# Optimization experiments

Hardware: AMD Instinct MI355X
Metric: run time of the kernel (lower is better)

The kernel has to match this reference:

```python
import jax, jax.numpy as jnp
import numpy as np

EMBED_DIM = 1024
NUM_HEADS = 16
HEAD_DIM = EMBED_DIM // NUM_HEADS
R = 8
ALPHA = 32
SCALING = ALPHA / R


def setup_inputs() -> dict:
    key = jax.random.key(0)
    ks = jax.random.split(key, 12)
    d = EMBED_DIM
    s = 1.0 / np.sqrt(d)
    inp = {
        "x": jax.random.normal(ks[0], (4, 2048, d), dtype=jnp.float32),
        # base linear weights (torch layout: [out, in]) and biases
        "Wq": jax.random.normal(ks[1], (d, d), dtype=jnp.float32) * s,
        "bq": jax.random.normal(ks[2], (d,), dtype=jnp.float32) * s,
        "Wk": jax.random.normal(ks[3], (d, d), dtype=jnp.float32) * s,
        "bk": jax.random.normal(ks[4], (d,), dtype=jnp.float32) * s,
        "Wv": jax.random.normal(ks[5], (d, d), dtype=jnp.float32) * s,
        "bv": jax.random.normal(ks[6], (d,), dtype=jnp.float32) * s,
        "Wo": jax.random.normal(ks[7], (d, d), dtype=jnp.float32) * s,
        "bo": jax.random.normal(ks[8], (d,), dtype=jnp.float32) * s,
        # LoRA adapters for q and v: A [r, in], B [out, r]
        "Aq": jax.random.normal(ks[9], (R, d), dtype=jnp.float32) * s,
        "Bq": jnp.zeros((d, R), dtype=jnp.float32),
        "Av": jax.random.normal(ks[10], (R, d), dtype=jnp.float32) * s,
        "Bv": jnp.zeros((d, R), dtype=jnp.float32),
    }
    return inp


def _lora_linear(x, W, b, A, Bm):
    # base: x @ W.T + b ; lora: scaling * (x @ A.T) @ B.T
    return x @ W.T + b + SCALING * ((x @ A.T) @ Bm.T)


def reference(x, Wq, bq, Wk, bk, Wv, bv, Wo, bo, Aq, Bq, Av, Bv):
    B, T, C = x.shape
    H, D = NUM_HEADS, HEAD_DIM
    q = _lora_linear(x, Wq, bq, Aq, Bq)
    k = x @ Wk.T + bk
    v = _lora_linear(x, Wv, bv, Av, Bv)
    # [B, T, C] -> [B, H, T, D]
    q = q.reshape(B, T, H, D).transpose(0, 2, 1, 3)
    k = k.reshape(B, T, H, D).transpose(0, 2, 1, 3)
    v = v.reshape(B, T, H, D).transpose(0, 2, 1, 3)
    scores = jnp.einsum("bhqd,bhkd->bhqk", q, k) / np.sqrt(D).astype(np.float32)
    weights = jax.nn.softmax(scores, axis=-1)
    out = jnp.einsum("bhqk,bhkd->bhqd", weights, v)
    out = out.transpose(0, 2, 1, 3).reshape(B, T, C)
    return out @ Wo.T + bo
```

## Files before the change

### kernel.cpp

```cpp
#include <hip/hip_runtime.h>
#include <hip/hip_bf16.h>
#include <stdint.h>

namespace {
constexpr int kB = 4, kT = 2048, kC = 1024, kH = 16, kD = 64;
constexpr int kM = kB * kT;
constexpr int kR = 8;
constexpr float kScaling = 4.0f;
constexpr float kInvSqrtD = 0.125f;
}

typedef short short8 __attribute__((ext_vector_type(8)));
typedef float f32x4 __attribute__((ext_vector_type(4)));
typedef unsigned short ushort4v __attribute__((ext_vector_type(4)));
typedef unsigned short ushort8v __attribute__((ext_vector_type(8)));

__device__ inline uint32_t f32_to_bf16_rne(float f) {
  uint32_t u = __float_as_uint(f);
  return (u + 0x7fffu + ((u >> 16) & 1u)) >> 16;
}

__device__ inline void split4(const float4 v, ushort4v& h, ushort4v& l) {
  const float f[4] = {v.x, v.y, v.z, v.w};
#pragma unroll
  for (int j = 0; j < 4; ++j) {
    const uint32_t hb = f32_to_bf16_rne(f[j]);
    const float hf = __uint_as_float(hb << 16);
    const uint32_t lb = f32_to_bf16_rne(f[j] - hf);
    h[j] = (unsigned short)hb;
    l[j] = (unsigned short)lb;
  }
}

__device__ inline short8 pack8(ushort4v a, ushort4v b) {
  short8 r;
  r[0] = (short)a[0]; r[1] = (short)a[1]; r[2] = (short)a[2]; r[3] = (short)a[3];
  r[4] = (short)b[0]; r[5] = (short)b[1]; r[6] = (short)b[2]; r[7] = (short)b[3];
  return r;
}

__global__ __launch_bounds__(256) void lora_xa_kernel(
    const float* __restrict__ x, const float* __restrict__ Aq,
    const float* __restrict__ Av, float* __restrict__ xa) {
  const int wave = threadIdx.x >> 6;
  const int lane = threadIdx.x & 63;
  const int row = (blockIdx.x << 2) + wave;
  const float4* xr = reinterpret_cast<const float4*>(x) + (size_t)row * (kC / 4);
  const float4* aq = reinterpret_cast<const float4*>(Aq);
  const float4* av = reinterpret_cast<const float4*>(Av);
  float acc[16];
#pragma unroll
  for (int r = 0; r < 16; ++r) acc[r] = 0.f;
#pragma unroll
  for (int jj = 0; jj < (kC / 4) / 64; ++jj) {
    const int j = lane + jj * 64;
    const float4 xv = xr[j];
#pragma unroll
    for (int r = 0; r < 8; ++r) {
      const float4 a = aq[r * (kC / 4) + j];
      acc[r] += xv.x * a.x + xv.y * a.y + xv.z * a.z + xv.w * a.w;
      const float4 b = av[r * (kC / 4) + j];
      acc[8 + r] += xv.x * b.x + xv.y * b.y + xv.z * b.z + xv.w * b.w;
    }
  }
#pragma unroll
  for (int r = 0; r < 16; ++r) {
    float v = acc[r];
#pragma unroll
    for (int off = 32; off > 0; off >>= 1) v += __shfl_xor(v, off, 64);
    if (lane == 0) xa[(size_t)row * 16 + r] = v;
  }
}

__global__ __launch_bounds__(256, 2) void gemm_bf16x3_kernel(
    const float* __restrict__ X, const float* __restrict__ W,
    const float* __restrict__ bias, const float* __restrict__ xa,
    const float* __restrict__ Bm, float* __restrict__ out,
    const int lora_sel ,
    const int out_mode) {
  constexpr int BK = 32;
  __shared__ __align__(16) unsigned char sA[128 * 128];
  __shared__ __align__(16) unsigned char sB[128 * 128];

  const int tid = threadIdx.x;
  const int m0 = blockIdx.y << 7;
  const int n0 = blockIdx.x << 7;
  const int wave = tid >> 6, lane = tid & 63;
  const int wr = wave >> 1, wc = wave & 1;
  const int lrow = lane & 15;
  const int lkg = lane >> 4;

  const int r0 = tid >> 3;
  const int c4 = (tid & 7) << 2;
  const float* xbase = X + (size_t)(m0 + r0) * kC + c4;
  const float* wbase = W + (size_t)(n0 + r0) * kC + c4;
  const int ch = c4 >> 3;
  const int slot = (c4 & 7) << 1;

  f32x4 acc[4][4];
#pragma unroll
  for (int a = 0; a < 4; ++a)
#pragma unroll
    for (int b = 0; b < 4; ++b) acc[a][b] = (f32x4){0.f, 0.f, 0.f, 0.f};

  float4 ga[4], gb[4];
#pragma unroll
  for (int i = 0; i < 4; ++i) {
    ga[i] = *reinterpret_cast<const float4*>(xbase + (size_t)i * 32 * kC);
    gb[i] = *reinterpret_cast<const float4*>(wbase + (size_t)i * 32 * kC);
  }

  for (int k0 = 0; k0 < kC; k0 += BK) {
#pragma unroll
    for (int i = 0; i < 4; ++i) {
      const int r = r0 + 32 * i;
      const int rbase = r * 128;
      const int s7 = r & 7;
      ushort4v ha, la, hb2, lb2;
      split4(ga[i], ha, la);
      split4(gb[i], hb2, lb2);
      *reinterpret_cast<ushort4v*>(&sA[rbase + ((ch ^ s7) << 4) + slot]) = ha;
      *reinterpret_cast<ushort4v*>(&sA[rbase + (((ch | 4) ^ s7) << 4) + slot]) = la;
      *reinterpret_cast<ushort4v*>(&sB[rbase + ((ch ^ s7) << 4) + slot]) = hb2;
      *reinterpret_cast<ushort4v*>(&sB[rbase + (((ch | 4) ^ s7) << 4) + slot]) = lb2;
    }
    __syncthreads();

    if (k0 + BK < kC) {
#pragma unroll
      for (int i = 0; i < 4; ++i) {
        ga[i] = *reinterpret_cast<const float4*>(xbase + (k0 + BK) + (size_t)i * 32 * kC);
        gb[i] = *reinterpret_cast<const float4*>(wbase + (k0 + BK) + (size_t)i * 32 * kC);
      }
    }

    short8 ah[4], al[4];
#pragma unroll
    for (int rb = 0; rb < 4; ++rb) {
      const int rA = wr * 64 + rb * 16 + lrow;
      ah[rb] = *reinterpret_cast<const short8*>(&sA[rA * 128 + ((lkg ^ (rA & 7)) << 4)]);
      al[rb] = *reinterpret_cast<const short8*>(&sA[rA * 128 + (((lkg | 4) ^ (rA & 7)) << 4)]);
    }
#pragma unroll
    for (int cb = 0; cb < 4; ++cb) {
      const int rB = wc * 64 + cb * 16 + lrow;
      const short8 bhf = *reinterpret_cast<const short8*>(&sB[rB * 128 + ((lkg ^ (rB & 7)) << 4)]);
      const short8 blf = *reinterpret_cast<const short8*>(&sB[rB * 128 + (((lkg | 4) ^ (rB & 7)) << 4)]);
#pragma unroll
      for (int rb = 0; rb < 4; ++rb) {
        acc[rb][cb] = __builtin_amdgcn_mfma_f32_16x16x32_bf16(ah[rb], bhf, acc[rb][cb], 0, 0, 0);
        acc[rb][cb] = __builtin_amdgcn_mfma_f32_16x16x32_bf16(ah[rb], blf, acc[rb][cb], 0, 0, 0);
        acc[rb][cb] = __builtin_amdgcn_mfma_f32_16x16x32_bf16(al[rb], bhf, acc[rb][cb], 0, 0, 0);
      }
    }
    __syncthreads();
  }

#pragma unroll
  for (int rb = 0; rb < 4; ++rb) {
    const int mbase = m0 + wr * 64 + rb * 16 + (lkg << 2);
    float la2[4][kR];
    if (lora_sel >= 0) {
#pragma unroll
      for (int i = 0; i < 4; ++i)
#pragma unroll
        for (int r = 0; r < kR; ++r)
          la2[i][r] = xa[(size_t)(mbase + i) * 16 + lora_sel + r];
    }
#pragma unroll
    for (int cb = 0; cb < 4; ++cb) {
      const int n = n0 + wc * 64 + cb * 16 + lrow;
      const float bi = bias[n];
      float vv[4];
#pragma unroll
      for (int i = 0; i < 4; ++i) {
        vv[i] = acc[rb][cb][i] + bi;
        if (lora_sel >= 0) {
          float lv = 0.f;
#pragma unroll
          for (int r = 0; r < kR; ++r)
            lv = fmaf(la2[i][r], Bm[(size_t)n * kR + r], lv);
          vv[i] += kScaling * lv;
        }
      }
      if (out_mode == 2) {
        const int bb_ = mbase >> 11;
        const int t0 = mbase & (kT - 1);
        const int hh = n >> 6;
        const int dd = n & (kD - 1);
        *reinterpret_cast<float4*>(
            out + (((size_t)bb_ * kH + hh) * kD + dd) * kT + t0) =
            make_float4(vv[0], vv[1], vv[2], vv[3]);
      } else if (out_mode == 1) {
#pragma unroll
        for (int i = 0; i < 4; ++i) {
          const int m = mbase + i;
          const int bb_ = m >> 11;
          const int t = m & (kT - 1);
          const int hh = n >> 6;
          const int dd = n & (kD - 1);
          out[(((size_t)bb_ * kH + hh) * kT + t) * kD + dd] = vv[i];
        }
      } else {
#pragma unroll
        for (int i = 0; i < 4; ++i)
          out[(size_t)(mbase + i) * kC + n] = vv[i];
      }
    }
  }
}

__global__ __launch_bounds__(256) void attn_mfma_kernel(
    const float* __restrict__ q, const float* __restrict__ k,
    const float* __restrict__ vT, float* __restrict__ ctx) {
  __shared__ __align__(16) unsigned char sKh[64 * 128];
  __shared__ __align__(16) unsigned char sKl[64 * 128];
  __shared__ __align__(16) unsigned char sVt[64 * 128];
  __shared__ __align__(16) unsigned char sP[128 * 128];

  const int tid = threadIdx.x;
  const int wave = tid >> 6, lane = tid & 63;
  const int lrow = lane & 15, lg = lane >> 4;
  const int bh = blockIdx.y;
  const int q0 = blockIdx.x << 7;
  const int b = bh >> 4, h = bh & 15;

  const float* qbh = q + (size_t)bh * kT * kD;
  const float* kbh = k + (size_t)bh * kT * kD;

  const int srow = tid >> 2;
  const int scq = (tid & 3) << 4;
  const float* kstage = kbh + (size_t)srow * kD + scq;
  const float* vstage = vT + ((size_t)bh * kD + srow) * kT + scq;

  short8 qh[2][2], ql[2][2];
#pragma unroll
  for (int qs = 0; qs < 2; ++qs)
#pragma unroll
    for (int d0 = 0; d0 < 2; ++d0) {
      const int qrow = q0 + wave * 32 + qs * 16 + lrow;
      const float* qp2 = qbh + (size_t)qrow * kD + d0 * 32 + lg * 8;
      float4 f0 = *reinterpret_cast<const float4*>(qp2);
      float4 f1 = *reinterpret_cast<const float4*>(qp2 + 4);
      f0.x *= kInvSqrtD; f0.y *= kInvSqrtD; f0.z *= kInvSqrtD; f0.w *= kInvSqrtD;
      f1.x *= kInvSqrtD; f1.y *= kInvSqrtD; f1.z *= kInvSqrtD; f1.w *= kInvSqrtD;
      ushort4v h0, l0, h1, l1;
      split4(f0, h0, l0);
      split4(f1, h1, l1);
      qh[qs][d0] = pack8(h0, h1);
      ql[qs][d0] = pack8(l0, l1);
    }

  f32x4 acc_o[2][4];
#pragma unroll
  for (int qs = 0; qs < 2; ++qs)
#pragma unroll
    for (int dr = 0; dr < 4; ++dr) acc_o[qs][dr] = (f32x4){0.f, 0.f, 0.f, 0.f};
  float m_i[2] = {-3.0e38f, -3.0e38f};
  float l_i[2] = {0.f, 0.f};

  constexpr int kNT = kT / 64;
  float4 kpre[4], vpre[4];
#pragma unroll
  for (int i = 0; i < 4; ++i) {
    kpre[i] = *reinterpret_cast<const float4*>(kstage + i * 4);
    vpre[i] = *reinterpret_cast<const float4*>(vstage + i * 4);
  }

  for (int kt = 0; kt < kNT; ++kt) {
    {
      const int s7k = srow & 7;
#pragma unroll
      for (int half = 0; half < 2; ++half) {
        ushort4v h0, l0, h1, l1;
        split4(kpre[2 * half], h0, l0);
        split4(kpre[2 * half + 1], h1, l1);
        const int chk = ((scq >> 3) + half) ^ s7k;
        *reinterpret_cast<ushort8v*>(&sKh[srow * 128 + (chk << 4)]) =
            (ushort8v){h0[0], h0[1], h0[2], h0[3], h1[0], h1[1], h1[2], h1[3]};
        *reinterpret_cast<ushort8v*>(&sKl[srow * 128 + (chk << 4)]) =
            (ushort8v){l0[0], l0[1], l0[2], l0[3], l1[0], l1[1], l1[2], l1[3]};
        ushort8v w;
        const float vf0[8] = {vpre[2 * half].x, vpre[2 * half].y,
                              vpre[2 * half].z, vpre[2 * half].w,
                              vpre[2 * half + 1].x, vpre[2 * half + 1].y,
                              vpre[2 * half + 1].z, vpre[2 * half + 1].w};
#pragma unroll
        for (int e = 0; e < 8; ++e) w[e] = (unsigned short)f32_to_bf16_rne(vf0[e]);
        *reinterpret_cast<ushort8v*>(&sVt[srow * 128 + (chk << 4)]) = w;
      }
    }
    __syncthreads();

    if (kt + 1 < kNT) {
      const int knext = (kt + 1) << 6;
#pragma unroll
      for (int i = 0; i < 4; ++i) {
        kpre[i] = *reinterpret_cast<const float4*>(kstage + (size_t)knext * kD + i * 4);
        vpre[i] = *reinterpret_cast<const float4*>(vstage + knext + i * 4);
      }
    }

    f32x4 acc_s[2][4];
#pragma unroll
    for (int qs = 0; qs < 2; ++qs)
#pragma unroll
      for (int kvr = 0; kvr < 4; ++kvr) acc_s[qs][kvr] = (f32x4){0.f, 0.f, 0.f, 0.f};
#pragma unroll
    for (int d0 = 0; d0 < 2; ++d0) {
#pragma unroll
      for (int kvr = 0; kvr < 4; ++kvr) {
        const int rk = kvr * 16 + lrow;
        const int byt = rk * 128 + ((((d0 << 2) + lg) ^ (rk & 7)) << 4);
        const short8 khf = *reinterpret_cast<const short8*>(&sKh[byt]);
        const short8 klf = *reinterpret_cast<const short8*>(&sKl[byt]);
#pragma unroll
        for (int qs = 0; qs < 2; ++qs) {
          acc_s[qs][kvr] = __builtin_amdgcn_mfma_f32_16x16x32_bf16(khf, qh[qs][d0], acc_s[qs][kvr], 0, 0, 0);
          acc_s[qs][kvr] = __builtin_amdgcn_mfma_f32_16x16x32_bf16(khf, ql[qs][d0], acc_s[qs][kvr], 0, 0, 0);
          acc_s[qs][kvr] = __builtin_amdgcn_mfma_f32_16x16x32_bf16(klf, qh[qs][d0], acc_s[qs][kvr], 0, 0, 0);
        }
      }
    }

#pragma unroll
    for (int qs = 0; qs < 2; ++qs) {
      float mx = acc_s[qs][0][0];
#pragma unroll
      for (int kvr = 0; kvr < 4; ++kvr)
#pragma unroll
        for (int i = 0; i < 4; ++i) mx = fmaxf(mx, acc_s[qs][kvr][i]);
      mx = fmaxf(mx, __shfl_xor(mx, 16, 64));
      mx = fmaxf(mx, __shfl_xor(mx, 32, 64));
      const float mnew = fmaxf(m_i[qs], mx);
      const float alpha = __expf(m_i[qs] - mnew);
      m_i[qs] = mnew;
      const int prow = wave * 32 + qs * 16 + lrow;
      const int p7 = prow & 7;
      float rs = 0.f;
#pragma unroll
      for (int kvr = 0; kvr < 4; ++kvr) {
        ushort4v pu;
#pragma unroll
        for (int i = 0; i < 4; ++i) {
          const float pv = __expf(acc_s[qs][kvr][i] - mnew);
          rs += pv;
          pu[i] = (unsigned short)f32_to_bf16_rne(pv);
        }
        const int chunk = ((kvr << 1) + (lg >> 1)) ^ p7;
        *reinterpret_cast<ushort4v*>(&sP[prow * 128 + (chunk << 4) + ((lg & 1) << 3)]) = pu;
      }
      rs += __shfl_xor(rs, 16, 64);
      rs += __shfl_xor(rs, 32, 64);
      l_i[qs] = l_i[qs] * alpha + rs;
#pragma unroll
      for (int dr = 0; dr < 4; ++dr)
#pragma unroll
        for (int i = 0; i < 4; ++i) acc_o[qs][dr][i] *= alpha;
    }
    __builtin_amdgcn_sched_barrier(0);

#pragma unroll
    for (int ks = 0; ks < 2; ++ks) {
      short8 pf[2];
#pragma unroll
      for (int qs = 0; qs < 2; ++qs) {
        const int prow = wave * 32 + qs * 16 + lrow;
        pf[qs] = *reinterpret_cast<const short8*>(
            &sP[prow * 128 + ((((ks << 2) + lg) ^ (prow & 7)) << 4)]);
      }
#pragma unroll
      for (int dr = 0; dr < 4; ++dr) {
        const int rv = dr * 16 + lrow;
        const short8 vf = *reinterpret_cast<const short8*>(
            &sVt[rv * 128 + ((((ks << 2) + lg) ^ (rv & 7)) << 4)]);
        acc_o[0][dr] = __builtin_amdgcn_mfma_f32_16x16x32_bf16(vf, pf[0], acc_o[0][dr], 0, 0, 0);
        acc_o[1][dr] = __builtin_amdgcn_mfma_f32_16x16x32_bf16(vf, pf[1], acc_o[1][dr], 0, 0, 0);
      }
    }
    __syncthreads();
  }

#pragma unroll
  for (int qs = 0; qs < 2; ++qs) {
    const float inv = 1.0f / l_i[qs];
    const int qq = q0 + wave * 32 + qs * 16 + lrow;
    float* op = ctx + ((size_t)b * kT + qq) * kC + (h << 6);
#pragma unroll
    for (int dr = 0; dr < 4; ++dr) {
      const float4 o4 = make_float4(acc_o[qs][dr][0] * inv, acc_o[qs][dr][1] * inv,
                                    acc_o[qs][dr][2] * inv, acc_o[qs][dr][3] * inv);
      *reinterpret_cast<float4*>(op + dr * 16 + (lg << 2)) = o4;
    }
  }
}

extern "C" void kernel_launch(void* const* d_in, const int* in_sizes, int n_in,
                              void* d_out, int out_size, void* d_ws, size_t ws_size,
                              hipStream_t stream) {
  const float* x  = (const float*)d_in[0];
  const float* Wq = (const float*)d_in[1];
  const float* bq = (const float*)d_in[2];
  const float* Wk = (const float*)d_in[3];
  const float* bk = (const float*)d_in[4];
  const float* Wv = (const float*)d_in[5];
  const float* bv = (const float*)d_in[6];
  const float* Wo = (const float*)d_in[7];
  const float* bo = (const float*)d_in[8];
  const float* Aq = (const float*)d_in[9];
  const float* Bq = (const float*)d_in[10];
  const float* Av = (const float*)d_in[11];
  const float* Bv = (const float*)d_in[12];
  float* out = (float*)d_out;

  float* ws = (float*)d_ws;
  float* qb  = ws;
  float* kb  = qb  + (size_t)kM * kC;
  float* vbT = kb  + (size_t)kM * kC;
  float* ctx = vbT + (size_t)kM * kC;
  float* xa  = ctx + (size_t)kM * kC;

  hipLaunchKernelGGL(lora_xa_kernel, dim3(kM / 4), dim3(256), 0, stream,
                     x, Aq, Av, xa);

  const dim3 gg(kC / 128, kM / 128);
  hipLaunchKernelGGL(gemm_bf16x3_kernel, gg, dim3(256), 0, stream,
                     x, Wq, bq, xa, Bq, qb, 0, 1);
  hipLaunchKernelGGL(gemm_bf16x3_kernel, gg, dim3(256), 0, stream,
                     x, Wk, bk, nullptr, nullptr, kb, -1, 1);
  hipLaunchKernelGGL(gemm_bf16x3_kernel, gg, dim3(256), 0, stream,
                     x, Wv, bv, xa, Bv, vbT, 8, 2);

  hipLaunchKernelGGL(attn_mfma_kernel, dim3(kT / 128, kB * kH), dim3(256), 0, stream,
                     qb, kb, vbT, ctx);

  hipLaunchKernelGGL(gemm_bf16x3_kernel, gg, dim3(256), 0, stream,
                     ctx, Wo, bo, nullptr, nullptr, out, -1, 0);
}
```

Measured before the change: 641.1 us.

## Pre-split operands into bf16 hi/lo planes and store intermediates as bf16

Adds a pack kernel that splits x and all four weight matrices into bf16 high/low planes once per call. The GEMMs and attention then load those planes directly instead of converting fp32 tiles inside their main loops. Q/K/V and the attention context are written as bf16 planes, which halves or keeps intermediate traffic and removes in-loop splitting. The softmax is folded into exp2 with the log2e factor baked into the Q scale, and P is packed with hardware bf16 conversions. The cost is extra pack passes over x and the weights, plus a larger workspace.

Measured after the change: 710.5 us. 1.11x slower.

```diff
diff --git a/kernel.cpp b/kernel.cpp
--- a/kernel.cpp
+++ b/kernel.cpp
@@ -7,36 +7,54 @@
 constexpr int kM = kB * kT;
 constexpr int kR = 8;
 constexpr float kScaling = 4.0f;
-constexpr float kInvSqrtD = 0.125f;
+constexpr float kQScale = 0.125f * 1.4426950408889634f;
 }
 
 typedef short short8 __attribute__((ext_vector_type(8)));
 typedef float f32x4 __attribute__((ext_vector_type(4)));
 typedef unsigned short ushort4v __attribute__((ext_vector_type(4)));
 typedef unsigned short ushort8v __attribute__((ext_vector_type(8)));
-
-__device__ inline uint32_t f32_to_bf16_rne(float f) {
-  uint32_t u = __float_as_uint(f);
-  return (u + 0x7fffu + ((u >> 16) & 1u)) >> 16;
-}
-
-__device__ inline void split4(const float4 v, ushort4v& h, ushort4v& l) {
-  const float f[4] = {v.x, v.y, v.z, v.w};
-#pragma unroll
-  for (int j = 0; j < 4; ++j) {
-    const uint32_t hb = f32_to_bf16_rne(f[j]);
-    const float hf = __uint_as_float(hb << 16);
-    const uint32_t lb = f32_to_bf16_rne(f[j] - hf);
-    h[j] = (unsigned short)hb;
-    l[j] = (unsigned short)lb;
-  }
-}
-
-__device__ inline short8 pack8(ushort4v a, ushort4v b) {
-  short8 r;
-  r[0] = (short)a[0]; r[1] = (short)a[1]; r[2] = (short)a[2]; r[3] = (short)a[3];
-  r[4] = (short)b[0]; r[5] = (short)b[1]; r[6] = (short)b[2]; r[7] = (short)b[3];
-  return r;
+typedef unsigned int uint2v __attribute__((ext_vector_type(2)));
+
+__device__ inline unsigned short bf16_bits(float f) {
+  __hip_bfloat16 h = __float2bfloat16(f);
+  unsigned short u;
+  __builtin_memcpy(&u, &h, 2);
+  return u;
+}
+__device__ inline float bits_f(unsigned short u) {
+  return __uint_as_float((uint32_t)u << 16);
+}
+__device__ inline void split1(float f, unsigned short& h, unsigned short& l) {
+  h = bf16_bits(f);
+  l = bf16_bits(f - bits_f(h));
+}
+__device__ inline uint32_t cvtpk2(float a, float b) {
+  __hip_bfloat162 h2 = __float22bfloat162_rn(float2{a, b});
+  uint32_t u;
+  __builtin_memcpy(&u, &h2, 4);
+  return u;
+}
+
+__global__ __launch_bounds__(256) void pack_kernel(
+    const float* __restrict__ s, unsigned short* __restrict__ hp,
+    unsigned short* __restrict__ lp, int n4) {
+  int i = blockIdx.x * 256 + threadIdx.x;
+  const int stride = gridDim.x * 256;
+  for (; i < n4; i += stride) {
+    const float4 v = reinterpret_cast<const float4*>(s)[i];
+    const float f[4] = {v.x, v.y, v.z, v.w};
+    ushort4v h, l;
+#pragma unroll
+    for (int j = 0; j < 4; ++j) {
+      unsigned short hb, lb;
+      split1(f[j], hb, lb);
+      h[j] = hb;
+      l[j] = lb;
+    }
+    reinterpret_cast<ushort4v*>(hp)[i] = h;
+    reinterpret_cast<ushort4v*>(lp)[i] = l;
+  }
 }
 
 __global__ __launch_bounds__(256) void lora_xa_kernel(
@@ -72,12 +90,14 @@
   }
 }
 
-__global__ __launch_bounds__(256, 2) void gemm_bf16x3_kernel(
-    const float* __restrict__ X, const float* __restrict__ W,
+__global__ __launch_bounds__(256, 2) void gemm_planes_kernel(
+    const unsigned short* __restrict__ Ah_g, const unsigned short* __restrict__ Al_g,
+    const unsigned short* __restrict__ Bh_g, const unsigned short* __restrict__ Bl_g,
     const float* __restrict__ bias, const float* __restrict__ xa,
-    const float* __restrict__ Bm, float* __restrict__ out,
-    const int lora_sel ,
-    const int out_mode) {
+    const float* __restrict__ Bm,
+    unsigned short* __restrict__ o16a, unsigned short* __restrict__ o16b,
+    float* __restrict__ o32,
+    const int lora_sel, const int out_mode, const float out_scale) {
   constexpr int BK = 32;
   __shared__ __align__(16) unsigned char sA[128 * 128];
   __shared__ __align__(16) unsigned char sB[128 * 128];
@@ -90,12 +110,12 @@
   const int lrow = lane & 15;
   const int lkg = lane >> 4;
 
-  const int r0 = tid >> 3;
-  const int c4 = (tid & 7) << 2;
-  const float* xbase = X + (size_t)(m0 + r0) * kC + c4;
-  const float* wbase = W + (size_t)(n0 + r0) * kC + c4;
-  const int ch = c4 >> 3;
-  const int slot = (c4 & 7) << 1;
+  const int srow = tid >> 1;
+  const int sc0 = (tid & 1) << 1;
+  const unsigned short* pa_h = Ah_g + (size_t)(m0 + srow) * kC + sc0 * 8;
+  const unsigned short* pa_l = Al_g + (size_t)(m0 + srow) * kC + sc0 * 8;
+  const unsigned short* pb_h = Bh_g + (size_t)(n0 + srow) * kC + sc0 * 8;
+  const unsigned short* pb_l = Bl_g + (size_t)(n0 + srow) * kC + sc0 * 8;
 
   f32x4 acc[4][4];
 #pragma unroll
@@ -103,34 +123,36 @@
 #pragma unroll
     for (int b = 0; b < 4; ++b) acc[a][b] = (f32x4){0.f, 0.f, 0.f, 0.f};
 
-  float4 ga[4], gb[4];
-#pragma unroll
-  for (int i = 0; i < 4; ++i) {
-    ga[i] = *reinterpret_cast<const float4*>(xbase + (size_t)i * 32 * kC);
-    gb[i] = *reinterpret_cast<const float4*>(wbase + (size_t)i * 32 * kC);
+  ushort8v rah[2], ral[2], rbh[2], rbl[2];
+#pragma unroll
+  for (int j = 0; j < 2; ++j) {
+    rah[j] = *reinterpret_cast<const ushort8v*>(pa_h + j * 8);
+    ral[j] = *reinterpret_cast<const ushort8v*>(pa_l + j * 8);
+    rbh[j] = *reinterpret_cast<const ushort8v*>(pb_h + j * 8);
+    rbl[j] = *reinterpret_cast<const ushort8v*>(pb_l + j * 8);
   }
 
   for (int k0 = 0; k0 < kC; k0 += BK) {
-#pragma unroll
-    for (int i = 0; i < 4; ++i) {
-      const int r = r0 + 32 * i;
-      const int rbase = r * 128;
-      const int s7 = r & 7;
-      ushort4v ha, la, hb2, lb2;
-      split4(ga[i], ha, la);
-      split4(gb[i], hb2, lb2);
-      *reinterpret_cast<ushort4v*>(&sA[rbase + ((ch ^ s7) << 4) + slot]) = ha;
-      *reinterpret_cast<ushort4v*>(&sA[rbase + (((ch | 4) ^ s7) << 4) + slot]) = la;
-      *reinterpret_cast<ushort4v*>(&sB[rbase + ((ch ^ s7) << 4) + slot]) = hb2;
-      *reinterpret_cast<ushort4v*>(&sB[rbase + (((ch | 4) ^ s7) << 4) + slot]) = lb2;
+    const int rbase = srow * 128;
+    const int s7 = srow & 7;
+#pragma unroll
+    for (int j = 0; j < 2; ++j) {
+      const int c = sc0 + j;
+      *reinterpret_cast<ushort8v*>(&sA[rbase + ((c ^ s7) << 4)]) = rah[j];
+      *reinterpret_cast<ushort8v*>(&sA[rbase + (((c | 4) ^ s7) << 4)]) = ral[j];
+      *reinterpret_cast<ushort8v*>(&sB[rbase + ((c ^ s7) << 4)]) = rbh[j];
+      *reinterpret_cast<ushort8v*>(&sB[rbase + (((c | 4) ^ s7) << 4)]) = rbl[j];
     }
     __syncthreads();
 
     if (k0 + BK < kC) {
-#pragma unroll
-      for (int i = 0; i < 4; ++i) {
-        ga[i] = *reinterpret_cast<const float4*>(xbase + (k0 + BK) + (size_t)i * 32 * kC);
-        gb[i] = *reinterpret_cast<const float4*>(wbase + (k0 + BK) + (size_t)i * 32 * kC);
+      const int kn = k0 + BK;
+#pragma unroll
+      for (int j = 0; j < 2; ++j) {
+        rah[j] = *reinterpret_cast<const ushort8v*>(pa_h + kn + j * 8);
+        ral[j] = *reinterpret_cast<const ushort8v*>(pa_l + kn + j * 8);
+        rbh[j] = *reinterpret_cast<const ushort8v*>(pb_h + kn + j * 8);
+        rbl[j] = *reinterpret_cast<const ushort8v*>(pb_l + kn + j * 8);
       }
     }
 
@@ -182,37 +204,45 @@
             lv = fmaf(la2[i][r], Bm[(size_t)n * kR + r], lv);
           vv[i] += kScaling * lv;
         }
-      }
-      if (out_mode == 2) {
+        vv[i] *= out_scale;
+      }
+      if (out_mode == 1) {
         const int bb_ = mbase >> 11;
         const int t0 = mbase & (kT - 1);
         const int hh = n >> 6;
         const int dd = n & (kD - 1);
-        *reinterpret_cast<float4*>(
-            out + (((size_t)bb_ * kH + hh) * kD + dd) * kT + t0) =
-            make_float4(vv[0], vv[1], vv[2], vv[3]);
-      } else if (out_mode == 1) {
 #pragma unroll
         for (int i = 0; i < 4; ++i) {
-          const int m = mbase + i;
-          const int bb_ = m >> 11;
-          const int t = m & (kT - 1);
-          const int hh = n >> 6;
-          const int dd = n & (kD - 1);
-          out[(((size_t)bb_ * kH + hh) * kT + t) * kD + dd] = vv[i];
+          const size_t off = (((size_t)bb_ * kH + hh) * kT + t0 + i) * kD + dd;
+          unsigned short hb, lb;
+          split1(vv[i], hb, lb);
+          o16a[off] = hb;
+          o16b[off] = lb;
         }
+      } else if (out_mode == 2) {
+        const int bb_ = mbase >> 11;
+        const int t0 = mbase & (kT - 1);
+        const int hh = n >> 6;
+        const int dd = n & (kD - 1);
+        ushort4v w;
+#pragma unroll
+        for (int i = 0; i < 4; ++i) w[i] = bf16_bits(vv[i]);
+        *reinterpret_cast<ushort4v*>(
+            o16a + (((size_t)bb_ * kH + hh) * kD + dd) * kT + t0) = w;
       } else {
 #pragma unroll
         for (int i = 0; i < 4; ++i)
-          out[(size_t)(mbase + i) * kC + n] = vv[i];
+          o32[(size_t)(mbase + i) * kC + n] = vv[i];
       }
     }
   }
 }
 
 __global__ __launch_bounds__(256) void attn_mfma_kernel(
-    const float* __restrict__ q, const float* __restrict__ k,
-    const float* __restrict__ vT, float* __restrict__ ctx) {
+    const unsigned short* __restrict__ Qh, const unsigned short* __restrict__ Ql,
+    const unsigned short* __restrict__ Kh_g, const unsigned short* __restrict__ Kl_g,
+    const unsigned short* __restrict__ Vt_g,
+    unsigned short* __restrict__ ctx_h, unsigned short* __restrict__ ctx_l) {
   __shared__ __align__(16) unsigned char sKh[64 * 128];
   __shared__ __align__(16) unsigned char sKl[64 * 128];
   __shared__ __align__(16) unsigned char sVt[64 * 128];
@@ -225,31 +255,22 @@
   const int q0 = blockIdx.x << 7;
   const int b = bh >> 4, h = bh & 15;
 
-  const float* qbh = q + (size_t)bh * kT * kD;
-  const float* kbh = k + (size_t)bh * kT * kD;
+  short8 qh[2][2], ql[2][2];
+#pragma unroll
+  for (int qs = 0; qs < 2; ++qs)
+#pragma unroll
+    for (int d0 = 0; d0 < 2; ++d0) {
+      const size_t off =
+          ((size_t)bh * kT + q0 + wave * 32 + qs * 16 + lrow) * kD + d0 * 32 + lg * 8;
+      qh[qs][d0] = *reinterpret_cast<const short8*>(Qh + off);
+      ql[qs][d0] = *reinterpret_cast<const short8*>(Ql + off);
+    }
 
   const int srow = tid >> 2;
-  const int scq = (tid & 3) << 4;
-  const float* kstage = kbh + (size_t)srow * kD + scq;
-  const float* vstage = vT + ((size_t)bh * kD + srow) * kT + scq;
-
-  short8 qh[2][2], ql[2][2];
-#pragma unroll
-  for (int qs = 0; qs < 2; ++qs)
-#pragma unroll
-    for (int d0 = 0; d0 < 2; ++d0) {
-      const int qrow = q0 + wave * 32 + qs * 16 + lrow;
-      const float* qp2 = qbh + (size_t)qrow * kD + d0 * 32 + lg * 8;
-      float4 f0 = *reinterpret_cast<const float4*>(qp2);
-      float4 f1 = *reinterpret_cast<const float4*>(qp2 + 4);
-      f0.x *= kInvSqrtD; f0.y *= kInvSqrtD; f0.z *= kInvSqrtD; f0.w *= kInvSqrtD;
-      f1.x *= kInvSqrtD; f1.y *= kInvSqrtD; f1.z *= kInvSqrtD; f1.w *= kInvSqrtD;
-      ushort4v h0, l0, h1, l1;
-      split4(f0, h0, l0);
-      split4(f1, h1, l1);
-      qh[qs][d0] = pack8(h0, h1);
-      ql[qs][d0] = pack8(l0, l1);
-    }
+  const int sc0 = (tid & 3) << 1;
+  const unsigned short* khs = Kh_g + ((size_t)bh * kT + srow) * kD + sc0 * 8;
+  const unsigned short* kls = Kl_g + ((size_t)bh * kT + srow) * kD + sc0 * 8;
+  const unsigned short* vts = Vt_g + ((size_t)bh * kD + srow) * kT + sc0 * 8;
 
   f32x4 acc_o[2][4];
 #pragma unroll
@@ -260,44 +281,36 @@
   float l_i[2] = {0.f, 0.f};
 
   constexpr int kNT = kT / 64;
-  float4 kpre[4], vpre[4];
-#pragma unroll
-  for (int i = 0; i < 4; ++i) {
-    kpre[i] = *reinterpret_cast<const float4*>(kstage + i * 4);
-    vpre[i] = *reinterpret_cast<const float4*>(vstage + i * 4);
+  ushort8v kph[2], kpl[2], vpv[2];
+#pragma unroll
+  for (int j = 0; j < 2; ++j) {
+    kph[j] = *reinterpret_cast<const ushort8v*>(khs + j * 8);
+    kpl[j] = *reinterpret_cast<const ushort8v*>(kls + j * 8);
+    vpv[j] = *reinterpret_cast<const ushort8v*>(vts + j * 8);
   }
 
   for (int kt = 0; kt < kNT; ++kt) {
     {
-      const int s7k = srow & 7;
-#pragma unroll
-      for (int half = 0; half < 2; ++half) {
-        ushort4v h0, l0, h1, l1;
-        split4(kpre[2 * half], h0, l0);
-        split4(kpre[2 * half + 1], h1, l1);
-        const int chk = ((scq >> 3) + half) ^ s7k;
-        *reinterpret_cast<ushort8v*>(&sKh[srow * 128 + (chk << 4)]) =
-            (ushort8v){h0[0], h0[1], h0[2], h0[3], h1[0], h1[1], h1[2], h1[3]};
-        *reinterpret_cast<ushort8v*>(&sKl[srow * 128 + (chk << 4)]) =
-            (ushort8v){l0[0], l0[1], l0[2], l0[3], l1[0], l1[1], l1[2], l1[3]};
-        ushort8v w;
-        const float vf0[8] = {vpre[2 * half].x, vpre[2 * half].y,
-                              vpre[2 * half].z, vpre[2 * half].w,
-                              vpre[2 * half + 1].x, vpre[2 * half + 1].y,
-                              vpre[2 * half + 1].z, vpre[2 * half + 1].w};
-#pragma unroll
-        for (int e = 0; e < 8; ++e) w[e] = (unsigned short)f32_to_bf16_rne(vf0[e]);
-        *reinterpret_cast<ushort8v*>(&sVt[srow * 128 + (chk << 4)]) = w;
+      const int rb2 = srow * 128;
+      const int s7 = srow & 7;
+#pragma unroll
+      for (int j = 0; j < 2; ++j) {
+        const int c = sc0 + j;
+        *reinterpret_cast<ushort8v*>(&sKh[rb2 + ((c ^ s7) << 4)]) = kph[j];
+        *reinterpret_cast<ushort8v*>(&sKl[rb2 + ((c ^ s7) << 4)]) = kpl[j];
+        *reinterpret_cast<ushort8v*>(&sVt[rb2 + ((c ^ s7) << 4)]) = vpv[j];
       }
     }
     __syncthreads();
 
     if (kt + 1 < kNT) {
-      const int knext = (kt + 1) << 6;
-#pragma unroll
-      for (int i = 0; i < 4; ++i) {
-        kpre[i] = *reinterpret_cast<const float4*>(kstage + (size_t)knext * kD + i * 4);
-        vpre[i] = *reinterpret_cast<const float4*>(vstage + knext + i * 4);
+      const size_t koffK = (size_t)(kt + 1) * 64 * kD;
+      const int koffV = (kt + 1) * 64;
+#pragma unroll
+      for (int j = 0; j < 2; ++j) {
+        kph[j] = *reinterpret_cast<const ushort8v*>(khs + koffK + j * 8);
+        kpl[j] = *reinterpret_cast<const ushort8v*>(kls + koffK + j * 8);
+        vpv[j] = *reinterpret_cast<const ushort8v*>(vts + koffV + j * 8);
       }
     }
 
@@ -333,22 +346,24 @@
       mx = fmaxf(mx, __shfl_xor(mx, 16, 64));
       mx = fmaxf(mx, __shfl_xor(mx, 32, 64));
       const float mnew = fmaxf(m_i[qs], mx);
-      const float alpha = __expf(m_i[qs] - mnew);
+      const float alpha = __builtin_exp2f(m_i[qs] - mnew);
       m_i[qs] = mnew;
       const int prow = wave * 32 + qs * 16 + lrow;
       const int p7 = prow & 7;
       float rs = 0.f;
 #pragma unroll
       for (int kvr = 0; kvr < 4; ++kvr) {
-        ushort4v pu;
+        float p[4];
 #pragma unroll
         for (int i = 0; i < 4; ++i) {
-          const float pv = __expf(acc_s[qs][kvr][i] - mnew);
-          rs += pv;
-          pu[i] = (unsigned short)f32_to_bf16_rne(pv);
+          p[i] = __builtin_exp2f(acc_s[qs][kvr][i] - mnew);
+          rs += p[i];
         }
+        uint2v pu;
+        pu[0] = cvtpk2(p[0], p[1]);
+        pu[1] = cvtpk2(p[2], p[3]);
         const int chunk = ((kvr << 1) + (lg >> 1)) ^ p7;
-        *reinterpret_cast<ushort4v*>(&sP[prow * 128 + (chunk << 4) + ((lg & 1) << 3)]) = pu;
+        *reinterpret_cast<uint2v*>(&sP[prow * 128 + (chunk << 4) + ((lg & 1) << 3)]) = pu;
       }
       rs += __shfl_xor(rs, 16, 64);
       rs += __shfl_xor(rs, 32, 64);
@@ -385,12 +400,19 @@
   for (int qs = 0; qs < 2; ++qs) {
     const float inv = 1.0f / l_i[qs];
     const int qq = q0 + wave * 32 + qs * 16 + lrow;
-    float* op = ctx + ((size_t)b * kT + qq) * kC + (h << 6);
+    const size_t base = ((size_t)b * kT + qq) * kC + (h << 6);
 #pragma unroll
     for (int dr = 0; dr < 4; ++dr) {
-      const float4 o4 = make_float4(acc_o[qs][dr][0] * inv, acc_o[qs][dr][1] * inv,
-                                    acc_o[qs][dr][2] * inv, acc_o[qs][dr][3] * inv);
-      *reinterpret_cast<float4*>(op + dr * 16 + (lg << 2)) = o4;
+      ushort4v wh, wl;
+#pragma unroll
+      for (int i = 0; i < 4; ++i) {
+        unsigned short hb, lb;
+        split1(acc_o[qs][dr][i] * inv, hb, lb);
+        wh[i] = hb;
+        wl[i] = lb;
+      }
+      *reinterpret_cast<ushort4v*>(ctx_h + base + dr * 16 + (lg << 2)) = wh;
+      *reinterpret_cast<ushort4v*>(ctx_l + base + dr * 16 + (lg << 2)) = wl;
     }
   }
 }
@@ -413,27 +435,45 @@
   const float* Bv = (const float*)d_in[12];
   float* out = (float*)d_out;
 
-  float* ws = (float*)d_ws;
-  float* qb  = ws;
-  float* kb  = qb  + (size_t)kM * kC;
-  float* vbT = kb  + (size_t)kM * kC;
-  float* ctx = vbT + (size_t)kM * kC;
-  float* xa  = ctx + (size_t)kM * kC;
-
-  hipLaunchKernelGGL(lora_xa_kernel, dim3(kM / 4), dim3(256), 0, stream,
-                     x, Aq, Av, xa);
+  constexpr size_t MP = (size_t)kM * kC;
+  constexpr size_t WP = (size_t)kC * kC;
+  unsigned short* w16 = (unsigned short*)d_ws;
+  unsigned short* Xh  = w16;
+  unsigned short* Xl  = Xh  + MP;
+  unsigned short* Wqh = Xl  + MP;
+  unsigned short* Wql = Wqh + WP;
+  unsigned short* Wkh = Wql + WP;
+  unsigned short* Wkl = Wkh + WP;
+  unsigned short* Wvh = Wkl + WP;
+  unsigned short* Wvl = Wvh + WP;
+  unsigned short* Woh = Wvl + WP;
+  unsigned short* Wol = Woh + WP;
+  unsigned short* Qh  = Wol + WP;
+  unsigned short* Ql  = Qh  + MP;
+  unsigned short* Kh  = Ql  + MP;
+  unsigned short* Kl  = Kh  + MP;
+  unsigned short* Vt  = Kl  + MP;
+  float* xa = (float*)(Vt + MP);
+
+  hipLaunchKernelGGL(pack_kernel, dim3(2048), dim3(256), 0, stream, x, Xh, Xl, (int)(MP / 4));
+  hipLaunchKernelGGL(pack_kernel, dim3(1024), dim3(256), 0, stream, Wq, Wqh, Wql, (int)(WP / 4));
+  hipLaunchKernelGGL(pack_kernel, dim3(1024), dim3(256), 0, stream, Wk, Wkh, Wkl, (int)(WP / 4));
+  hipLaunchKernelGGL(pack_kernel, dim3(1024), dim3(256), 0, stream, Wv, Wvh, Wvl, (int)(WP / 4));
+  hipLaunchKernelGGL(pack_kernel, dim3(1024), dim3(256), 0, stream, Wo, Woh, Wol, (int)(WP / 4));
+
+  hipLaunchKernelGGL(lora_xa_kernel, dim3(kM / 4), dim3(256), 0, stream, x, Aq, Av, xa);
 
   const dim3 gg(kC / 128, kM / 128);
-  hipLaunchKernelGGL(gemm_bf16x3_kernel, gg, dim3(256), 0, stream,
-                     x, Wq, bq, xa, Bq, qb, 0, 1);
-  hipLaunchKernelGGL(gemm_bf16x3_kernel, gg, dim3(256), 0, stream,
-                     x, Wk, bk, nullptr, nullptr, kb, -1, 1);
-  hipLaunchKernelGGL(gemm_bf16x3_kernel, gg, dim3(256), 0, stream,
-                     x, Wv, bv, xa, Bv, vbT, 8, 2);
+  hipLaunchKernelGGL(gemm_planes_kernel, gg, dim3(256), 0, stream,
+                     Xh, Xl, Wqh, Wql, bq, xa, Bq, Qh, Ql, nullptr, 0, 1, kQScale);
+  hipLaunchKernelGGL(gemm_planes_kernel, gg, dim3(256), 0, stream,
+                     Xh, Xl, Wkh, Wkl, bk, nullptr, nullptr, Kh, Kl, nullptr, -1, 1, 1.0f);
+  hipLaunchKernelGGL(gemm_planes_kernel, gg, dim3(256), 0, stream,
+                     Xh, Xl, Wvh, Wvl, bv, xa, Bv, Vt, nullptr, nullptr, 8, 2, 1.0f);
 
   hipLaunchKernelGGL(attn_mfma_kernel, dim3(kT / 128, kB * kH), dim3(256), 0, stream,
-                     qb, kb, vbT, ctx);
-
-  hipLaunchKernelGGL(gemm_bf16x3_kernel, gg, dim3(256), 0, stream,
-                     ctx, Wo, bo, nullptr, nullptr, out, -1, 0);
-}
+                     Qh, Ql, Kh, Kl, Vt, Xh, Xl);
+
+  hipLaunchKernelGGL(gemm_planes_kernel, gg, dim3(256), 0, stream,
+                     Xh, Xl, Woh, Wol, bo, nullptr, nullptr, nullptr, nullptr, out, -1, 0, 1.0f);
+}
```
